# Kernel tuning notes

Hardware: AMD Instinct MI355X
Metric: run time of the kernel (lower is better)

The kernel has to match this reference:

```python
import jax, jax.numpy as jnp
import numpy as np

B, D, K, NDIM = 4, 81, 2048, 4  # batch, feature dim, n mixture components, box coord dims


def setup_inputs() -> dict:
    key = jax.random.key(0)
    k1, k2, k3, k4 = jax.random.split(key, 4)
    x = jax.random.normal(k1, (B, D, K), dtype=jnp.float32)
    # mixture weights, positive and normalized over components
    pi = jax.nn.softmax(jax.random.normal(k2, (B, 1, K), dtype=jnp.float32), axis=2)
    # component means in [0,1] (normalized box coords)
    mu = jax.random.uniform(k3, (B, NDIM, K), dtype=jnp.float32)
    # positive scales
    sig = jax.random.uniform(k4, (B, NDIM, K), dtype=jnp.float32) * 0.1 + 0.01
    return {"x": x, "pi": pi, "mu": mu, "sig": sig}


def _cauchy_pdf(mu, sig, points):
    # mu, sig: (B, 1, NDIM, K); points: (B, P, NDIM, 1)
    d = points - mu
    return sig / (jnp.pi * (d * d + sig * sig))


def reference(x, pi, mu, sig):
    # points = mu.transpose(1,2): evaluate the mixture at each component mean
    points = jnp.transpose(mu, (0, 2, 1))            # (B, K, NDIM)
    comp = _cauchy_pdf(mu[:, None, :, :], sig[:, None, :, :],
                       points[:, :, :, None])        # (B, K, NDIM, K)
    comp = jnp.prod(comp, axis=2)                    # independent dims -> (B, K, K)
    lh = pi * comp                                   # pi (B,1,K) broadcasts over points
    coef = lh / jnp.sum(lh, axis=2, keepdims=True)   # normalize over components
    coef = jax.lax.stop_gradient(coef)               # coef_detach=True
    y = jnp.einsum('bdk,bkm->bdm', x, coef)          # torch.bmm(x, coef)
    return y
```

## Files before the change

kernel.cpp:

```cpp
#include <hip/hip_runtime.h>


typedef float v4f __attribute__((ext_vector_type(4)));
typedef float f32x4 __attribute__((ext_vector_type(4)));
typedef short bf16x8 __attribute__((ext_vector_type(8)));

namespace {
constexpr int BB = 4;
constexpr int DD = 81;
constexpr int KK = 2048;
constexpr int MROWS = 96;
constexpr float INV_PI4 = 1.0f / 97.40909103400243f;

constexpr size_t OFF_XBF = 0;
constexpr size_t OFF_RSP = (size_t)BB * MROWS * KK * 2;
}

__device__ __forceinline__ unsigned short f2bf(float f) {
    union { float f; unsigned int u; } v; v.f = f;
    unsigned int u = v.u;
    unsigned int r = (u + 0x7FFFu + ((u >> 16) & 1u)) >> 16;
    return (unsigned short)r;
}

__global__ __launch_bounds__(256) void prep_kernel(const float* __restrict__ x,
                                                   const float* __restrict__ pi_,
                                                   const float* __restrict__ mu,
                                                   const float* __restrict__ sig,
                                                   float* __restrict__ rowsumPart,
                                                   unsigned short* __restrict__ xbf) {
    __shared__ v4f   mush[256];
    __shared__ v4f   s2sh[256];
    __shared__ float csh[256];
    __shared__ float red[4][64];

    int blk = blockIdx.x;
    int b   = blk >> 8;
    int pc  = (blk & 255) >> 3;
    int ms  = blk & 7;
    int p0  = pc * 64;
    int m0  = ms * 256;
    int t   = threadIdx.x;
    int lane = t & 63, w = t >> 6;

    const float* mub = mu  + (size_t)b * 4 * KK;
    const float* sgb = sig + (size_t)b * 4 * KK;
    const float* pib = pi_ + (size_t)b * KK;

    {
        int m = m0 + t;
        v4f mm = {mub[m], mub[KK + m], mub[2 * KK + m], mub[3 * KK + m]};
        v4f sg = {sgb[m], sgb[KK + m], sgb[2 * KK + m], sgb[3 * KK + m]};
        mush[t] = mm;
        s2sh[t] = sg * sg;
        csh[t]  = pib[m] * ((sg.x * sg.y) * (sg.z * sg.w)) * INV_PI4;
    }
    int p = p0 + lane;
    v4f mp = {mub[p], mub[KK + p], mub[2 * KK + p], mub[3 * KK + p]};

    {
        int rembase = (blk & 255) * 768;
        const float* xb = x + (size_t)b * DD * KK;
#pragma unroll
        for (int k = 0; k < 3; ++k) {
            int rem = rembase + k * 256 + t;
            int d   = rem >> 11;
            int pp  = rem & 2047;
            float v = 0.f;
            if (d < DD) v = xb[(size_t)d * KK + pp];
            xbf[(size_t)b * MROWS * KK + rem] = f2bf(v);
        }
    }
    __syncthreads();

    float sum = 0.f;
#pragma unroll 4
    for (int i = 0; i < 64; ++i) {
        int mi = w * 64 + i;
        v4f d = mp - mush[mi];
        v4f q = d * d + s2sh[mi];
        float den = (q.x * q.y) * (q.z * q.w);
        sum += csh[mi] * __builtin_amdgcn_rcpf(den);
    }

    red[w][lane] = sum;
    __syncthreads();
    if (t < 64)
        rowsumPart[((size_t)(b * 8 + ms)) * KK + p0 + t] =
            red[0][t] + red[1][t] + red[2][t] + red[3][t];
}

__global__ __launch_bounds__(512) void gemm_kernel(const float* __restrict__ pi_,
                                                   const float* __restrict__ mu,
                                                   const float* __restrict__ sig,
                                                   const float* __restrict__ rowsumPart,
                                                   const unsigned short* __restrict__ xbf,
                                                   float* __restrict__ out) {
    __shared__ __align__(16) char smem[49152];
    v4f*   mus  = (v4f*)smem;
    float* invs = (float*)(smem + 32768);
    f32x4 (*red)[6][64] = (f32x4 (*)[6][64])smem;

    int t = threadIdx.x;
    int w = t >> 6, lane = t & 63;
    int r = lane & 15, q = lane >> 4;
    int b  = blockIdx.y;
    int m0 = blockIdx.x * 32;

    const float* mub = mu  + (size_t)b * 4 * KK;
    const float* sgb = sig + (size_t)b * 4 * KK;
    const float* rspb = rowsumPart + (size_t)b * 8 * KK;

    for (int i = t; i < KK; i += 512)
        mus[i] = (v4f){mub[i], mub[KK + i], mub[2 * KK + i], mub[3 * KK + i]};
    for (int i = t; i < KK; i += 512) {
        float s = 0.f;
#pragma unroll
        for (int sidx = 0; sidx < 8; ++sidx) s += rspb[(size_t)sidx * KK + i];
        invs[i] = __builtin_amdgcn_rcpf(s);
    }

    int mA = m0 + r, mB = m0 + 16 + r;
    v4f mmA = {mub[mA], mub[KK + mA], mub[2 * KK + mA], mub[3 * KK + mA]};
    v4f sgA = {sgb[mA], sgb[KK + mA], sgb[2 * KK + mA], sgb[3 * KK + mA]};
    v4f s2A = sgA * sgA;
    float cA = pi_[(size_t)b * KK + mA] * ((sgA.x * sgA.y) * (sgA.z * sgA.w)) * INV_PI4;
    v4f mmB = {mub[mB], mub[KK + mB], mub[2 * KK + mB], mub[3 * KK + mB]};
    v4f sgB = {sgb[mB], sgb[KK + mB], sgb[2 * KK + mB], sgb[3 * KK + mB]};
    v4f s2B = sgB * sgB;
    float cB = pi_[(size_t)b * KK + mB] * ((sgB.x * sgB.y) * (sgB.z * sgB.w)) * INV_PI4;

    const unsigned short* Abase = xbf + ((size_t)(b * MROWS + r)) * KK;

    f32x4 acc0[6], acc1[6];
#pragma unroll
    for (int i = 0; i < 6; ++i) { acc0[i] = (f32x4)0.f; acc1[i] = (f32x4)0.f; }

    __syncthreads();

    int pw = w * 256;
#pragma unroll
    for (int ks = 0; ks < 8; ++ks) {
        int pb = pw + ks * 32 + q * 8;
        bf16x8 Bf0, Bf1;
#pragma unroll
        for (int j = 0; j < 8; ++j) {
            v4f mp  = mus[pb + j];
            float iv = invs[pb + j];
            v4f d0 = mp - mmA;
            v4f q0 = d0 * d0 + s2A;
            float den0 = (q0.x * q0.y) * (q0.z * q0.w);
            Bf0[j] = (short)f2bf((cA * iv) * __builtin_amdgcn_rcpf(den0));
            v4f d1 = mp - mmB;
            v4f q1 = d1 * d1 + s2B;
            float den1 = (q1.x * q1.y) * (q1.z * q1.w);
            Bf1[j] = (short)f2bf((cB * iv) * __builtin_amdgcn_rcpf(den1));
        }
        bf16x8 Af[6];
#pragma unroll
        for (int Mt = 0; Mt < 6; ++Mt)
            Af[Mt] = *(const bf16x8*)(Abase + (size_t)Mt * 16 * KK + pb);
#pragma unroll
        for (int Mt = 0; Mt < 6; ++Mt) {
            acc0[Mt] = __builtin_amdgcn_mfma_f32_16x16x32_bf16(Af[Mt], Bf0, acc0[Mt], 0, 0, 0);
            acc1[Mt] = __builtin_amdgcn_mfma_f32_16x16x32_bf16(Af[Mt], Bf1, acc1[Mt], 0, 0, 0);
        }
    }

    int col = t & 15;
    int dr  = t >> 4;
#pragma unroll
    for (int nt = 0; nt < 2; ++nt) {
        __syncthreads();
#pragma unroll
        for (int Mt = 0; Mt < 6; ++Mt)
            red[w][Mt][lane] = (nt == 0) ? acc0[Mt] : acc1[Mt];
        __syncthreads();
#pragma unroll
        for (int k = 0; k < 3; ++k) {
            int d = dr + 32 * k;
            if (d < DD) {
                int Mt  = d >> 4;
                int row = d & 15;
                int l   = (row >> 2) * 16 + col;
                int j   = row & 3;
                float s = 0.f;
#pragma unroll
                for (int ww = 0; ww < 8; ++ww) s += red[ww][Mt][l][j];
                out[((size_t)(b * DD + d)) * KK + m0 + nt * 16 + col] = s;
            }
        }
    }
}

extern "C" void kernel_launch(void* const* d_in, const int* in_sizes, int n_in,
                              void* d_out, int out_size, void* d_ws, size_t ws_size,
                              hipStream_t stream) {
    const float* x   = (const float*)d_in[0];
    const float* pi_ = (const float*)d_in[1];
    const float* mu  = (const float*)d_in[2];
    const float* sig = (const float*)d_in[3];
    float* out = (float*)d_out;

    unsigned short* xbf = (unsigned short*)((char*)d_ws + OFF_XBF);
    float* rowsumPart   = (float*)((char*)d_ws + OFF_RSP);

    prep_kernel<<<1024, 256, 0, stream>>>(x, pi_, mu, sig, rowsumPart, xbf);
    dim3 gg(KK / 32, BB);
    gemm_kernel<<<gg, 512, 0, stream>>>(pi_, mu, sig, rowsumPart, xbf, out);
}
```

Measured before the change: 92.08 us.

## Fuse prep and GEMM into one cooperative kernel with grid syncs

Merges the row-sum prep kernel and the GEMM kernel into a single cooperative launch of 256 blocks. Each block computes its likelihood tile once, keeps it in registers, and writes column partial sums. Two grid-wide syncs then reduce those sums and broadcast the inverse. This removes the duplicated Cauchy evaluation and one kernel launch, and packs to bf16 with a hardware convert instruction. In exchange it adds grid-sync latency, needs many registers to hold 128 values per thread, and adds global traffic for the partial sums.

After: 157.5 us. +71.0%, slower.

```diff
diff --git a/kernel.cpp b/kernel.cpp
--- a/kernel.cpp
+++ b/kernel.cpp
@@ -1,4 +1,7 @@
 #include <hip/hip_runtime.h>
+#include <hip/hip_cooperative_groups.h>
+
+namespace cg = cooperative_groups;
 
 
 typedef float v4f __attribute__((ext_vector_type(4)));
@@ -12,8 +15,9 @@
 constexpr int MROWS = 96;
 constexpr float INV_PI4 = 1.0f / 97.40909103400243f;
 
-constexpr size_t OFF_XBF = 0;
-constexpr size_t OFF_RSP = (size_t)BB * MROWS * KK * 2;
+constexpr size_t OFF_XBF   = 0;
+constexpr size_t OFF_PARTS = (size_t)BB * MROWS * KK * 2;
+constexpr size_t OFF_RS    = OFF_PARTS + (size_t)BB * 64 * KK * 4;
 }
 
 __device__ __forceinline__ unsigned short f2bf(float f) {
@@ -23,102 +27,31 @@
     return (unsigned short)r;
 }
 
-__global__ __launch_bounds__(256) void prep_kernel(const float* __restrict__ x,
-                                                   const float* __restrict__ pi_,
-                                                   const float* __restrict__ mu,
-                                                   const float* __restrict__ sig,
-                                                   float* __restrict__ rowsumPart,
-                                                   unsigned short* __restrict__ xbf) {
-    __shared__ v4f   mush[256];
-    __shared__ v4f   s2sh[256];
-    __shared__ float csh[256];
-    __shared__ float red[4][64];
-
-    int blk = blockIdx.x;
-    int b   = blk >> 8;
-    int pc  = (blk & 255) >> 3;
-    int ms  = blk & 7;
-    int p0  = pc * 64;
-    int m0  = ms * 256;
-    int t   = threadIdx.x;
-    int lane = t & 63, w = t >> 6;
-
-    const float* mub = mu  + (size_t)b * 4 * KK;
-    const float* sgb = sig + (size_t)b * 4 * KK;
-    const float* pib = pi_ + (size_t)b * KK;
-
-    {
-        int m = m0 + t;
-        v4f mm = {mub[m], mub[KK + m], mub[2 * KK + m], mub[3 * KK + m]};
-        v4f sg = {sgb[m], sgb[KK + m], sgb[2 * KK + m], sgb[3 * KK + m]};
-        mush[t] = mm;
-        s2sh[t] = sg * sg;
-        csh[t]  = pib[m] * ((sg.x * sg.y) * (sg.z * sg.w)) * INV_PI4;
-    }
-    int p = p0 + lane;
-    v4f mp = {mub[p], mub[KK + p], mub[2 * KK + p], mub[3 * KK + p]};
-
-    {
-        int rembase = (blk & 255) * 768;
-        const float* xb = x + (size_t)b * DD * KK;
-#pragma unroll
-        for (int k = 0; k < 3; ++k) {
-            int rem = rembase + k * 256 + t;
-            int d   = rem >> 11;
-            int pp  = rem & 2047;
-            float v = 0.f;
-            if (d < DD) v = xb[(size_t)d * KK + pp];
-            xbf[(size_t)b * MROWS * KK + rem] = f2bf(v);
-        }
-    }
-    __syncthreads();
-
-    float sum = 0.f;
-#pragma unroll 4
-    for (int i = 0; i < 64; ++i) {
-        int mi = w * 64 + i;
-        v4f d = mp - mush[mi];
-        v4f q = d * d + s2sh[mi];
-        float den = (q.x * q.y) * (q.z * q.w);
-        sum += csh[mi] * __builtin_amdgcn_rcpf(den);
-    }
-
-    red[w][lane] = sum;
-    __syncthreads();
-    if (t < 64)
-        rowsumPart[((size_t)(b * 8 + ms)) * KK + p0 + t] =
-            red[0][t] + red[1][t] + red[2][t] + red[3][t];
-}
-
-__global__ __launch_bounds__(512) void gemm_kernel(const float* __restrict__ pi_,
-                                                   const float* __restrict__ mu,
-                                                   const float* __restrict__ sig,
-                                                   const float* __restrict__ rowsumPart,
-                                                   const unsigned short* __restrict__ xbf,
-                                                   float* __restrict__ out) {
-    __shared__ __align__(16) char smem[49152];
-    v4f*   mus  = (v4f*)smem;
+__global__ __launch_bounds__(512, 1) void fused_kernel(
+    const float* __restrict__ x, const float* __restrict__ pi_,
+    const float* __restrict__ mu, const float* __restrict__ sig,
+    float* __restrict__ parts, float* __restrict__ rs,
+    unsigned short* __restrict__ xbf, float* __restrict__ out) {
+    __shared__ __align__(16) char smem[50176];
+    v4f*  mus = (v4f*)smem;
+    float (*rsT)[16][33] = (float (*)[16][33])(smem + 32768);
+    float (*bsum)[33] = (float (*)[33])smem;
     float* invs = (float*)(smem + 32768);
     f32x4 (*red)[6][64] = (f32x4 (*)[6][64])smem;
 
     int t = threadIdx.x;
     int w = t >> 6, lane = t & 63;
     int r = lane & 15, q = lane >> 4;
-    int b  = blockIdx.y;
-    int m0 = blockIdx.x * 32;
+    int bid = blockIdx.x;
+    int b  = bid >> 6;
+    int mt = bid & 63;
+    int m0 = mt * 32;
 
     const float* mub = mu  + (size_t)b * 4 * KK;
     const float* sgb = sig + (size_t)b * 4 * KK;
-    const float* rspb = rowsumPart + (size_t)b * 8 * KK;
 
     for (int i = t; i < KK; i += 512)
         mus[i] = (v4f){mub[i], mub[KK + i], mub[2 * KK + i], mub[3 * KK + i]};
-    for (int i = t; i < KK; i += 512) {
-        float s = 0.f;
-#pragma unroll
-        for (int sidx = 0; sidx < 8; ++sidx) s += rspb[(size_t)sidx * KK + i];
-        invs[i] = __builtin_amdgcn_rcpf(s);
-    }
 
     int mA = m0 + r, mB = m0 + 16 + r;
     v4f mmA = {mub[mA], mub[KK + mA], mub[2 * KK + mA], mub[3 * KK + mA]};
@@ -130,31 +63,100 @@
     v4f s2B = sgB * sgB;
     float cB = pi_[(size_t)b * KK + mB] * ((sgB.x * sgB.y) * (sgB.z * sgB.w)) * INV_PI4;
 
-    const unsigned short* Abase = xbf + ((size_t)(b * MROWS + r)) * KK;
-
-    f32x4 acc0[6], acc1[6];
-#pragma unroll
-    for (int i = 0; i < 6; ++i) { acc0[i] = (f32x4)0.f; acc1[i] = (f32x4)0.f; }
-
+    {
+        const float* xb = x + (size_t)b * DD * KK;
+        unsigned short* xo = xbf + (size_t)b * MROWS * KK;
+        int rembase = (bid & 63) * 3072;
+#pragma unroll
+        for (int k = 0; k < 6; ++k) {
+            int rem = rembase + k * 512 + t;
+            int d   = rem >> 11;
+            int pp  = rem & 2047;
+            float v = (d < DD) ? xb[(size_t)d * KK + pp] : 0.f;
+            xo[rem] = f2bf(v);
+        }
+    }
     __syncthreads();
 
+    float lh0[8][8], lh1[8][8];
     int pw = w * 256;
+    int pl = lane & 31, h = lane >> 5;
 #pragma unroll
     for (int ks = 0; ks < 8; ++ks) {
         int pb = pw + ks * 32 + q * 8;
-        bf16x8 Bf0, Bf1;
 #pragma unroll
         for (int j = 0; j < 8; ++j) {
-            v4f mp  = mus[pb + j];
-            float iv = invs[pb + j];
+            v4f mp = mus[pb + j];
             v4f d0 = mp - mmA;
             v4f q0 = d0 * d0 + s2A;
             float den0 = (q0.x * q0.y) * (q0.z * q0.w);
-            Bf0[j] = (short)f2bf((cA * iv) * __builtin_amdgcn_rcpf(den0));
+            float l0 = cA * __builtin_amdgcn_rcpf(den0);
             v4f d1 = mp - mmB;
             v4f q1 = d1 * d1 + s2B;
             float den1 = (q1.x * q1.y) * (q1.z * q1.w);
-            Bf1[j] = (short)f2bf((cB * iv) * __builtin_amdgcn_rcpf(den1));
+            float l1 = cB * __builtin_amdgcn_rcpf(den1);
+            lh0[ks][j] = l0;
+            lh1[ks][j] = l1;
+            rsT[w][r][q * 8 + j] = l0 + l1;
+        }
+        float s = 0.f;
+#pragma unroll
+        for (int k = 0; k < 8; ++k) s += rsT[w][h * 8 + k][pl];
+        s += __shfl_xor(s, 32);
+        if (h == 0)
+            parts[((size_t)(b * 64 + mt)) * KK + pw + ks * 32 + pl] = s;
+    }
+
+    cg::this_grid().sync();
+
+    {
+        int ps = t & 31;
+        int g  = t >> 5;
+        int slot = bid * 32 + ps;
+        int b2 = slot >> 11, p2 = slot & 2047;
+        float s = 0.f;
+#pragma unroll
+        for (int i = 0; i < 4; ++i)
+            s += parts[((size_t)(b2 * 64 + g * 4 + i)) * KK + p2];
+        bsum[g][ps] = s;
+        __syncthreads();
+        if (t < 32) {
+            float tot = 0.f;
+#pragma unroll
+            for (int g2 = 0; g2 < 16; ++g2) tot += bsum[g2][t];
+            rs[(size_t)b2 * KK + p2] = tot;
+        }
+    }
+
+    cg::this_grid().sync();
+
+    {
+        const float* rsb = rs + (size_t)b * KK;
+        for (int i = t; i < KK; i += 512)
+            invs[i] = __builtin_amdgcn_rcpf(rsb[i]);
+    }
+    __syncthreads();
+
+    const unsigned short* Abase = xbf + ((size_t)(b * MROWS + r)) * KK;
+    f32x4 acc0[6], acc1[6];
+#pragma unroll
+    for (int i = 0; i < 6; ++i) { acc0[i] = (f32x4)0.f; acc1[i] = (f32x4)0.f; }
+
+#pragma unroll
+    for (int ks = 0; ks < 8; ++ks) {
+        int pb = pw + ks * 32 + q * 8;
+        f32x4 iv0 = *(const f32x4*)&invs[pb];
+        f32x4 iv1 = *(const f32x4*)&invs[pb + 4];
+        float iv[8] = {iv0.x, iv0.y, iv0.z, iv0.w, iv1.x, iv1.y, iv1.z, iv1.w};
+        union { int i4[4]; bf16x8 v; } u0, u1;
+#pragma unroll
+        for (int d2 = 0; d2 < 4; ++d2) {
+            float a0 = lh0[ks][2 * d2]     * iv[2 * d2];
+            float a1 = lh0[ks][2 * d2 + 1] * iv[2 * d2 + 1];
+            float b0 = lh1[ks][2 * d2]     * iv[2 * d2];
+            float b1 = lh1[ks][2 * d2 + 1] * iv[2 * d2 + 1];
+            asm("v_cvt_pk_bf16_f32 %0, %1, %2" : "=v"(u0.i4[d2]) : "v"(a0), "v"(a1));
+            asm("v_cvt_pk_bf16_f32 %0, %1, %2" : "=v"(u1.i4[d2]) : "v"(b0), "v"(b1));
         }
         bf16x8 Af[6];
 #pragma unroll
@@ -162,8 +164,8 @@
             Af[Mt] = *(const bf16x8*)(Abase + (size_t)Mt * 16 * KK + pb);
 #pragma unroll
         for (int Mt = 0; Mt < 6; ++Mt) {
-            acc0[Mt] = __builtin_amdgcn_mfma_f32_16x16x32_bf16(Af[Mt], Bf0, acc0[Mt], 0, 0, 0);
-            acc1[Mt] = __builtin_amdgcn_mfma_f32_16x16x32_bf16(Af[Mt], Bf1, acc1[Mt], 0, 0, 0);
+            acc0[Mt] = __builtin_amdgcn_mfma_f32_16x16x32_bf16(Af[Mt], u0.v, acc0[Mt], 0, 0, 0);
+            acc1[Mt] = __builtin_amdgcn_mfma_f32_16x16x32_bf16(Af[Mt], u1.v, acc1[Mt], 0, 0, 0);
         }
     }
 
@@ -203,9 +205,11 @@
     float* out = (float*)d_out;
 
     unsigned short* xbf = (unsigned short*)((char*)d_ws + OFF_XBF);
-    float* rowsumPart   = (float*)((char*)d_ws + OFF_RSP);
-
-    prep_kernel<<<1024, 256, 0, stream>>>(x, pi_, mu, sig, rowsumPart, xbf);
-    dim3 gg(KK / 32, BB);
-    gemm_kernel<<<gg, 512, 0, stream>>>(pi_, mu, sig, rowsumPart, xbf, out);
-}
+    float* parts        = (float*)((char*)d_ws + OFF_PARTS);
+    float* rs           = (float*)((char*)d_ws + OFF_RS);
+
+    void* args[] = {(void*)&x, (void*)&pi_, (void*)&mu, (void*)&sig,
+                    (void*)&parts, (void*)&rs, (void*)&xbf, (void*)&out};
+    hipLaunchCooperativeKernel(reinterpret_cast<void*>(fused_kernel),
+                               dim3(256), dim3(512), args, 0, stream);
+}
```
